# Optimization experiments

Measured on AMD Instinct MI355X. Metric: run time of the kernel, lower is better.

Reference implementation:

```python
import jax, jax.numpy as jnp
import numpy as np

B, N, M = 8, 8192, 2048
C, CP = 256, 256          # num_features, num_features_prev
D1, D2 = 256, 256         # layer_dims
BN_EPS = 1e-5


def setup_inputs() -> dict:
    key = jax.random.key(0)
    ks = jax.random.split(key, 8)
    return {
        "xyz": jax.random.normal(ks[0], (B, N, 3), dtype=jnp.float32),
        "xyz_prev": jax.random.normal(ks[1], (B, M, 3), dtype=jnp.float32),
        "features": jax.random.normal(ks[2], (B, C, N), dtype=jnp.float32),
        "features_prev": jax.random.normal(ks[3], (B, CP, M), dtype=jnp.float32),
        "w1": jax.random.normal(ks[4], (D1, C + CP), dtype=jnp.float32) * 0.02,
        "b1": jnp.zeros((D1,), dtype=jnp.float32),
        "g1": jnp.ones((D1,), dtype=jnp.float32),
        "beta1": jnp.zeros((D1,), dtype=jnp.float32),
        "w2": jax.random.normal(ks[5], (D2, D1), dtype=jnp.float32) * 0.02,
        "b2": jnp.zeros((D2,), dtype=jnp.float32),
        "g2": jnp.ones((D2,), dtype=jnp.float32),
        "beta2": jnp.zeros((D2,), dtype=jnp.float32),
    }


def _three_nn(unknown, known):
    # squared pairwise distances via GEMM form: [B, n, m]
    sq_u = jnp.sum(unknown * unknown, axis=-1)          # [B, n]
    sq_k = jnp.sum(known * known, axis=-1)              # [B, m]
    d2 = sq_u[:, :, None] + sq_k[:, None, :] - 2.0 * jnp.einsum(
        "bnd,bmd->bnm", unknown, known)
    neg_top, idx = jax.lax.top_k(-d2, 3)                # 3 smallest, ascending
    dist = jnp.sqrt(jnp.maximum(-neg_top, 0.0))         # [B, n, 3]
    return dist, idx


def _three_interpolate(features, idx, weight):
    # features [B, c, m], idx [B, n, 3], weight [B, n, 3] -> [B, c, n]
    gathered = jax.vmap(lambda f, i: f[:, i])(features, idx)  # [B, c, n, 3]
    return jnp.einsum("bcnk,bnk->bcn", gathered, weight)


def _bn_relu(x, gamma, beta):
    # training-mode BatchNorm1d over (batch, points), biased variance
    mean = jnp.mean(x, axis=(0, 2), keepdims=True)
    var = jnp.var(x, axis=(0, 2), keepdims=True)
    xh = (x - mean) * jax.lax.rsqrt(var + BN_EPS)
    return jnp.maximum(xh * gamma[None, :, None] + beta[None, :, None], 0.0)


def reference(xyz, xyz_prev, features, features_prev,
              w1, b1, g1, beta1, w2, b2, g2, beta2):
    dist, idx = _three_nn(xyz, xyz_prev)
    inv = 1.0 / (dist + 1e-8)
    weights = inv / jnp.sum(inv, axis=2, keepdims=True)           # [B, n, 3]
    new_features = _three_interpolate(features_prev, idx, weights)  # [B, cp, n]
    x = jnp.concatenate([new_features, features], axis=1)           # [B, cp+c, n]
    x = _bn_relu(jnp.einsum("oi,bin->bon", w1, x) + b1[None, :, None], g1, beta1)
    x = _bn_relu(jnp.einsum("oi,bin->bon", w2, x) + b2[None, :, None], g2, beta2)
    return x
```

## Files before the change

kernel.cpp:

```cpp
#include <hip/hip_runtime.h>

#define BDIM 8
#define NPTS 8192
#define MPTS 2048
#define NCHUNK 8
#define CHSZ 256
#define NSAMP 65536.0f
#define PITCH 40

typedef __attribute__((ext_vector_type(8))) short bf16x8;
typedef __attribute__((ext_vector_type(4))) float f32x4;

static __device__ __forceinline__ unsigned short f2bf(float f) {
  unsigned int x = __float_as_uint(f);
  x += 0x7FFFu + ((x >> 16) & 1u);
  return (unsigned short)(x >> 16);
}
static __device__ __forceinline__ float bf2f(unsigned short u) {
  return __uint_as_float(((unsigned int)u) << 16);
}

__global__ __launch_bounds__(256, 8)
void prep_kernel(const float* __restrict__ xyz, const float* __restrict__ xyz_prev,
                 float4* __restrict__ pd, int4* __restrict__ pi,
                 const float* __restrict__ features, unsigned short* __restrict__ Xf,
                 const float* __restrict__ features_prev, unsigned short* __restrict__ fpT,
                 const float* __restrict__ w1, const float* __restrict__ w2,
                 unsigned short* __restrict__ w1b, unsigned short* __restrict__ w2b) {
  __shared__ __align__(16) char smem[9216];
  const int tid = threadIdx.x;
  const int grp = blockIdx.x / 31, slot = blockIdx.x % 31;

  if (slot < 8) {
    const int id = grp*8 + slot;
    float4* pk = (float4*)smem;
    const int ch = (id >> 5) & 7, b = id >> 8;
    const int mbase = ch*CHSZ;
    {
      const int j = mbase + tid;
      float x = xyz_prev[((size_t)b*MPTS + j)*3 + 0];
      float y = xyz_prev[((size_t)b*MPTS + j)*3 + 1];
      float z = xyz_prev[((size_t)b*MPTS + j)*3 + 2];
      float s = __fadd_rn(__fadd_rn(__fmul_rn(x,x), __fmul_rn(y,y)), __fmul_rn(z,z));
      pk[tid] = make_float4(x, y, z, s);
    }
    __syncthreads();
    const int n = (id & 31)*256 + tid;
    const size_t qoff = ((size_t)b*NPTS + n)*3;
    const float qx = xyz[qoff], qy = xyz[qoff+1], qz = xyz[qoff+2];
    const float squ = __fadd_rn(__fadd_rn(__fmul_rn(qx,qx), __fmul_rn(qy,qy)), __fmul_rn(qz,qz));

    float d0 = 3.4e38f, d1 = 3.4e38f, d2v = 3.4e38f;
    int j0 = 0, j1 = 0, j2 = 0;
    for (int m = 0; m < CHSZ; m += 16) {
      float dd[16];
      #pragma unroll
      for (int u = 0; u < 16; ++u) {
        const float4 p = pk[m + u];
        float dot = __fadd_rn(__fadd_rn(__fmul_rn(qx,p.x), __fmul_rn(qy,p.y)), __fmul_rn(qz,p.z));
        dd[u] = __fsub_rn(__fadd_rn(squ, p.w), __fmul_rn(2.0f, dot));
      }
      float mn = dd[0];
      #pragma unroll
      for (int u = 1; u < 16; ++u) mn = fminf(mn, dd[u]);
      if (mn < d2v) {
        #pragma unroll
        for (int u = 0; u < 16; ++u) {
          const float v = dd[u];
          if (v < d2v) {
            if (v < d1) {
              d2v = d1; j2 = j1;
              if (v < d0) { d1 = d0; j1 = j0; d0 = v; j0 = mbase + m + u; }
              else        { d1 = v;  j1 = mbase + m + u; }
            } else { d2v = v; j2 = mbase + m + u; }
          }
        }
      }
    }
    const size_t q = (size_t)b*NPTS + n;
    pd[(size_t)ch*(BDIM*NPTS) + q] = make_float4(d0, d1, d2v, 0.f);
    pi[(size_t)ch*(BDIM*NPTS) + q] = make_int4(j0, j1, j2, 0);

  } else if (slot < 24) {
    const int id = grp*16 + (slot - 8);
    unsigned short (*St)[72] = (unsigned short(*)[72])smem;
    const int n0 = (id & 127)*64, c0 = ((id >> 7) & 3)*64, b = id >> 9;
    const int cl = tid >> 2;
    #pragma unroll
    for (int i = 0; i < 4; ++i) {
      int nl = (tid & 3)*16 + i*4;
      float4 v = *(const float4*)&features[((size_t)(b*256 + c0 + cl))*NPTS + n0 + nl];
      St[cl][nl]   = f2bf(v.x); St[cl][nl+1] = f2bf(v.y);
      St[cl][nl+2] = f2bf(v.z); St[cl][nl+3] = f2bf(v.w);
    }
    __syncthreads();
    #pragma unroll
    for (int i = 0; i < 2; ++i) {
      int u = tid + i*256;
      int nl = u >> 3, c8 = (u & 7)*8;
      unsigned short tmp[8];
      #pragma unroll
      for (int j = 0; j < 8; ++j) tmp[j] = St[c8 + j][nl];
      *(uint4*)&Xf[((size_t)(b*NPTS + n0 + nl))*256 + c0 + c8] = *(uint4*)tmp;
    }

  } else if (slot < 28) {
    const int id = grp*4 + (slot - 24);
    unsigned short (*St)[72] = (unsigned short(*)[72])smem;
    const int n0 = (id & 31)*64, c0 = ((id >> 5) & 3)*64, b = id >> 7;
    const int cl = tid >> 2;
    #pragma unroll
    for (int i = 0; i < 4; ++i) {
      int nl = (tid & 3)*16 + i*4;
      float4 v = *(const float4*)&features_prev[((size_t)(b*256 + c0 + cl))*MPTS + n0 + nl];
      St[cl][nl]   = f2bf(v.x); St[cl][nl+1] = f2bf(v.y);
      St[cl][nl+2] = f2bf(v.z); St[cl][nl+3] = f2bf(v.w);
    }
    __syncthreads();
    #pragma unroll
    for (int i = 0; i < 2; ++i) {
      int u = tid + i*256;
      int nl = u >> 3, c8 = (u & 7)*8;
      unsigned short tmp[8];
      #pragma unroll
      for (int j = 0; j < 8; ++j) tmp[j] = St[c8 + j][nl];
      *(uint4*)&fpT[((size_t)(b*MPTS + n0 + nl))*256 + c0 + c8] = *(uint4*)tmp;
    }

  } else {
    const int id = grp*3 + (slot - 28);
    const int t = id*256 + tid;
    if (t < 131072) w1b[t] = f2bf(w1[t]);
    else            w2b[t - 131072] = f2bf(w2[t - 131072]);
  }
}

__global__ __launch_bounds__(256)
void nn_merge_kernel(const float4* __restrict__ pd, const int4* __restrict__ pi,
                     int* __restrict__ idx_out, float* __restrict__ wgt_out) {
  const size_t q = (size_t)blockIdx.x*256 + threadIdx.x;
  float d0 = 3.4e38f, d1 = 3.4e38f, d2v = 3.4e38f;
  int j0 = 0, j1 = 0, j2 = 0;
  #pragma unroll
  for (int c = 0; c < NCHUNK; ++c) {
    const float4 dv = pd[(size_t)c*(BDIM*NPTS) + q];
    const int4   iv = pi[(size_t)c*(BDIM*NPTS) + q];
    const float dl[3] = {dv.x, dv.y, dv.z};
    const int   jl[3] = {iv.x, iv.y, iv.z};
    #pragma unroll
    for (int t = 0; t < 3; ++t) {
      const float v = dl[t]; const int j = jl[t];
      if (v < d2v) {
        if (v < d1) {
          d2v = d1; j2 = j1;
          if (v < d0) { d1 = d0; j1 = j0; d0 = v; j0 = j; }
          else        { d1 = v;  j1 = j; }
        } else { d2v = v; j2 = j; }
      }
    }
  }
  const float s0 = sqrtf(fmaxf(d0, 0.f));
  const float s1 = sqrtf(fmaxf(d1, 0.f));
  const float s2 = sqrtf(fmaxf(d2v, 0.f));
  const float i0 = 1.f/(s0 + 1e-8f), i1 = 1.f/(s1 + 1e-8f), i2 = 1.f/(s2 + 1e-8f);
  const float sum = i0 + i1 + i2;
  idx_out[q*3] = j0; idx_out[q*3+1] = j1; idx_out[q*3+2] = j2;
  wgt_out[q*3] = i0/sum; wgt_out[q*3+1] = i1/sum; wgt_out[q*3+2] = i2/sum;
}

__global__ __launch_bounds__(512)
void gemm1_fused_kernel(const unsigned short* __restrict__ W,
                        const unsigned short* __restrict__ Xf,
                        const unsigned short* __restrict__ fpT,
                        const int* __restrict__ idx, const float* __restrict__ wgt,
                        const float* __restrict__ bias,
                        unsigned short* __restrict__ Y, float* __restrict__ part) {
  __shared__ __align__(16) unsigned short Ws[256*PITCH];
  __shared__ __align__(16) unsigned short Xs[128*PITCH];
  __shared__ float lsum[256], lsq[256];
  const int tid = threadIdx.x;
  const int b = blockIdx.y, n0 = blockIdx.x*128;
  const int row = tid >> 2, seg = tid & 3;

  if (tid < 256) { lsum[tid] = 0.f; lsq[tid] = 0.f; }

  const size_t p = ((size_t)b*NPTS + n0 + row)*3;
  const int   i0 = idx[p],  i1 = idx[p+1],  i2 = idx[p+2];
  const float w0 = wgt[p],  w1 = wgt[p+1],  w2 = wgt[p+2];
  const unsigned short* fb  = fpT + (size_t)b*MPTS*256;
  const unsigned short* Xfb = Xf  + ((size_t)(b*NPTS + n0) + row)*256;

  uint4 wv0 = *(const uint4*)&W[(size_t)row*512 + seg*8];
  uint4 wv1 = *(const uint4*)&W[(size_t)(row+128)*512 + seg*8];
  uint4 xv;
  {
    const int k0 = seg*8;
    uint4 a0 = *(const uint4*)&fb[(size_t)i0*256 + k0];
    uint4 a1 = *(const uint4*)&fb[(size_t)i1*256 + k0];
    uint4 a2 = *(const uint4*)&fb[(size_t)i2*256 + k0];
    const unsigned short* u0 = (const unsigned short*)&a0;
    const unsigned short* u1 = (const unsigned short*)&a1;
    const unsigned short* u2 = (const unsigned short*)&a2;
    unsigned short r[8];
    #pragma unroll
    for (int j = 0; j < 8; ++j)
      r[j] = f2bf(bf2f(u0[j])*w0 + bf2f(u1[j])*w1 + bf2f(u2[j])*w2);
    xv = *(uint4*)r;
  }

  f32x4 acc[4][4];
  #pragma unroll
  for (int i = 0; i < 4; ++i)
    #pragma unroll
    for (int j = 0; j < 4; ++j) acc[i][j] = (f32x4){0.f,0.f,0.f,0.f};

  const int lane = tid & 63, l16 = lane & 15, quad = lane >> 4;
  const int wave = tid >> 6, wo = wave >> 1, wn = wave & 1;

  for (int kt = 0; kt < 16; ++kt) {
    __syncthreads();
    *(uint4*)&Ws[row*PITCH + seg*8]       = wv0;
    *(uint4*)&Ws[(row+128)*PITCH + seg*8] = wv1;
    *(uint4*)&Xs[row*PITCH + seg*8]       = xv;
    __syncthreads();
    if (kt + 1 < 16) {
      const int k0 = (kt+1)*32;
      wv0 = *(const uint4*)&W[(size_t)row*512 + k0 + seg*8];
      wv1 = *(const uint4*)&W[(size_t)(row+128)*512 + k0 + seg*8];
      const int kx = k0 + seg*8;
      if (kx < 256) {
        uint4 a0 = *(const uint4*)&fb[(size_t)i0*256 + kx];
        uint4 a1 = *(const uint4*)&fb[(size_t)i1*256 + kx];
        uint4 a2 = *(const uint4*)&fb[(size_t)i2*256 + kx];
        const unsigned short* u0 = (const unsigned short*)&a0;
        const unsigned short* u1 = (const unsigned short*)&a1;
        const unsigned short* u2 = (const unsigned short*)&a2;
        unsigned short r[8];
        #pragma unroll
        for (int j = 0; j < 8; ++j)
          r[j] = f2bf(bf2f(u0[j])*w0 + bf2f(u1[j])*w1 + bf2f(u2[j])*w2);
        xv = *(uint4*)r;
      } else {
        xv = *(const uint4*)&Xfb[kx - 256];
      }
    }
    bf16x8 af[4], bfr[4];
    #pragma unroll
    for (int to = 0; to < 4; ++to)
      af[to] = *(const bf16x8*)&Ws[(wo*64 + to*16 + l16)*PITCH + quad*8];
    #pragma unroll
    for (int tn = 0; tn < 4; ++tn)
      bfr[tn] = *(const bf16x8*)&Xs[(wn*64 + tn*16 + l16)*PITCH + quad*8];
    #pragma unroll
    for (int to = 0; to < 4; ++to)
      #pragma unroll
      for (int tn = 0; tn < 4; ++tn)
        acc[to][tn] = __builtin_amdgcn_mfma_f32_16x16x32_bf16(af[to], bfr[tn], acc[to][tn], 0, 0, 0);
  }

  #pragma unroll
  for (int to = 0; to < 4; ++to) {
    #pragma unroll
    for (int r = 0; r < 4; ++r) {
      const int o = wo*64 + to*16 + quad*4 + r;
      const float bv = bias[o];
      float ps = 0.f, qs = 0.f;
      #pragma unroll
      for (int tn = 0; tn < 4; ++tn) {
        float v = acc[to][tn][r] + bv;
        acc[to][tn][r] = v;
        ps += v; qs = fmaf(v, v, qs);
      }
      #pragma unroll
      for (int m = 1; m < 16; m <<= 1) { ps += __shfl_xor(ps, m); qs += __shfl_xor(qs, m); }
      if (l16 == 0) { atomicAdd(&lsum[o], ps); atomicAdd(&lsq[o], qs); }
    }
  }
  #pragma unroll
  for (int to = 0; to < 4; ++to)
    #pragma unroll
    for (int tn = 0; tn < 4; ++tn) {
      const int n = n0 + wn*64 + tn*16 + l16;
      const int o = wo*64 + to*16 + quad*4;
      unsigned int lo = (unsigned)f2bf(acc[to][tn][0]) | ((unsigned)f2bf(acc[to][tn][1]) << 16);
      unsigned int hi = (unsigned)f2bf(acc[to][tn][2]) | ((unsigned)f2bf(acc[to][tn][3]) << 16);
      *(uint2*)&Y[((size_t)(b*NPTS + n))*256 + o] = make_uint2(lo, hi);
    }
  __syncthreads();
  if (tid < 256) {
    const int blk = b*gridDim.x + blockIdx.x;
    part[(size_t)blk*512 + tid]       = lsum[tid];
    part[(size_t)blk*512 + 256 + tid] = lsq[tid];
  }
}

template<int KD, int MODE>
__global__ __launch_bounds__(512)
void gemm_t_kernel(const unsigned short* __restrict__ W, const unsigned short* __restrict__ X,
                   const float* __restrict__ bias, const float* __restrict__ scl,
                   const float* __restrict__ shf, unsigned short* __restrict__ Y,
                   float* __restrict__ part) {
  __shared__ __align__(16) unsigned short Ws[256*PITCH];
  __shared__ __align__(16) unsigned short Xs[128*PITCH];
  __shared__ float lsum[256], lsq[256];
  const int tid = threadIdx.x;
  const int b = blockIdx.y, n0 = blockIdx.x*128;
  const int row = tid >> 2, seg = tid & 3;
  const unsigned short* Xb = X + (size_t)(b*NPTS + n0)*KD;

  if (tid < 256) { lsum[tid] = 0.f; lsq[tid] = 0.f; }

  uint4 wv0 = *(const uint4*)&W[(size_t)row*KD + seg*8];
  uint4 wv1 = *(const uint4*)&W[(size_t)(row+128)*KD + seg*8];
  uint4 xv  = *(const uint4*)&Xb[(size_t)row*KD + seg*8];

  f32x4 acc[4][4];
  #pragma unroll
  for (int i = 0; i < 4; ++i)
    #pragma unroll
    for (int j = 0; j < 4; ++j) acc[i][j] = (f32x4){0.f,0.f,0.f,0.f};

  const int lane = tid & 63, l16 = lane & 15, quad = lane >> 4;
  const int wave = tid >> 6, wo = wave >> 1, wn = wave & 1;

  for (int kt = 0; kt < KD/32; ++kt) {
    __syncthreads();
    *(uint4*)&Ws[row*PITCH + seg*8]       = wv0;
    *(uint4*)&Ws[(row+128)*PITCH + seg*8] = wv1;
    if (MODE == 0) {
      *(uint4*)&Xs[row*PITCH + seg*8] = xv;
    } else {
      const int kc = kt*32 + seg*8;
      float4 s0 = *(const float4*)&scl[kc], s1 = *(const float4*)&scl[kc+4];
      float4 h0 = *(const float4*)&shf[kc], h1 = *(const float4*)&shf[kc+4];
      const unsigned short* xu = (const unsigned short*)&xv;
      unsigned short t[8];
      t[0] = f2bf(fmaxf(fmaf(bf2f(xu[0]), s0.x, h0.x), 0.f));
      t[1] = f2bf(fmaxf(fmaf(bf2f(xu[1]), s0.y, h0.y), 0.f));
      t[2] = f2bf(fmaxf(fmaf(bf2f(xu[2]), s0.z, h0.z), 0.f));
      t[3] = f2bf(fmaxf(fmaf(bf2f(xu[3]), s0.w, h0.w), 0.f));
      t[4] = f2bf(fmaxf(fmaf(bf2f(xu[4]), s1.x, h1.x), 0.f));
      t[5] = f2bf(fmaxf(fmaf(bf2f(xu[5]), s1.y, h1.y), 0.f));
      t[6] = f2bf(fmaxf(fmaf(bf2f(xu[6]), s1.z, h1.z), 0.f));
      t[7] = f2bf(fmaxf(fmaf(bf2f(xu[7]), s1.w, h1.w), 0.f));
      *(uint4*)&Xs[row*PITCH + seg*8] = *(uint4*)t;
    }
    __syncthreads();
    if (kt + 1 < KD/32) {
      const int k0 = (kt+1)*32;
      wv0 = *(const uint4*)&W[(size_t)row*KD + k0 + seg*8];
      wv1 = *(const uint4*)&W[(size_t)(row+128)*KD + k0 + seg*8];
      xv  = *(const uint4*)&Xb[(size_t)row*KD + k0 + seg*8];
    }
    bf16x8 af[4], bfr[4];
    #pragma unroll
    for (int to = 0; to < 4; ++to)
      af[to] = *(const bf16x8*)&Ws[(wo*64 + to*16 + l16)*PITCH + quad*8];
    #pragma unroll
    for (int tn = 0; tn < 4; ++tn)
      bfr[tn] = *(const bf16x8*)&Xs[(wn*64 + tn*16 + l16)*PITCH + quad*8];
    #pragma unroll
    for (int to = 0; to < 4; ++to)
      #pragma unroll
      for (int tn = 0; tn < 4; ++tn)
        acc[to][tn] = __builtin_amdgcn_mfma_f32_16x16x32_bf16(af[to], bfr[tn], acc[to][tn], 0, 0, 0);
  }

  #pragma unroll
  for (int to = 0; to < 4; ++to) {
    #pragma unroll
    for (int r = 0; r < 4; ++r) {
      const int o = wo*64 + to*16 + quad*4 + r;
      const float bv = bias[o];
      float p = 0.f, q = 0.f;
      #pragma unroll
      for (int tn = 0; tn < 4; ++tn) {
        float v = acc[to][tn][r] + bv;
        acc[to][tn][r] = v;
        p += v; q = fmaf(v, v, q);
      }
      #pragma unroll
      for (int m = 1; m < 16; m <<= 1) { p += __shfl_xor(p, m); q += __shfl_xor(q, m); }
      if (l16 == 0) { atomicAdd(&lsum[o], p); atomicAdd(&lsq[o], q); }
    }
  }
  #pragma unroll
  for (int to = 0; to < 4; ++to)
    #pragma unroll
    for (int tn = 0; tn < 4; ++tn) {
      const int n = n0 + wn*64 + tn*16 + l16;
      const int o = wo*64 + to*16 + quad*4;
      unsigned int lo = (unsigned)f2bf(acc[to][tn][0]) | ((unsigned)f2bf(acc[to][tn][1]) << 16);
      unsigned int hi = (unsigned)f2bf(acc[to][tn][2]) | ((unsigned)f2bf(acc[to][tn][3]) << 16);
      *(uint2*)&Y[((size_t)(b*NPTS + n))*256 + o] = make_uint2(lo, hi);
    }
  __syncthreads();
  if (tid < 256) {
    const int blk = b*gridDim.x + blockIdx.x;
    part[(size_t)blk*512 + tid]       = lsum[tid];
    part[(size_t)blk*512 + 256 + tid] = lsq[tid];
  }
}

__global__ __launch_bounds__(256)
void bn_reduce_kernel(const float* __restrict__ part, const float* __restrict__ g,
                      const float* __restrict__ beta, float* __restrict__ scl,
                      float* __restrict__ shf) {
  __shared__ float ls[4], lq[4];
  const int o = blockIdx.x;
  const int t = threadIdx.x;
  float s = part[(size_t)t*512 + o]        + part[(size_t)(t+256)*512 + o];
  float q = part[(size_t)t*512 + 256 + o]  + part[(size_t)(t+256)*512 + 256 + o];
  #pragma unroll
  for (int m = 1; m < 64; m <<= 1) { s += __shfl_xor(s, m); q += __shfl_xor(q, m); }
  const int w = t >> 6;
  if ((t & 63) == 0) { ls[w] = s; lq[w] = q; }
  __syncthreads();
  if (t == 0) {
    const float ss = ls[0] + ls[1] + ls[2] + ls[3];
    const float qq = lq[0] + lq[1] + lq[2] + lq[3];
    const float inv_n = 1.0f / NSAMP;
    const float mean = ss * inv_n;
    const float var  = qq * inv_n - mean*mean;
    const float sc = g[o] * rsqrtf(var + 1e-5f);
    scl[o] = sc;
    shf[o] = beta[o] - mean * sc;
  }
}

__global__ __launch_bounds__(256)
void bn2_t_kernel(const unsigned short* __restrict__ Yt, const float* __restrict__ scl,
                  const float* __restrict__ shf, float* __restrict__ out) {
  __shared__ __align__(16) unsigned short T[64][72];
  const int tid = threadIdx.x;
  const int n0 = blockIdx.x*64, o0 = blockIdx.y*64, b = blockIdx.z;
  #pragma unroll
  for (int i = 0; i < 2; ++i) {
    int u = tid + i*256;
    int nl = u >> 3, o8 = (u & 7)*8;
    uint4 v = *(const uint4*)&Yt[((size_t)(b*NPTS + n0 + nl))*256 + o0 + o8];
    *(uint4*)&T[nl][o8] = v;
  }
  __syncthreads();
  #pragma unroll
  for (int i = 0; i < 4; ++i) {
    int u = tid + i*256;
    int ol = u >> 4, n4 = (u & 15)*4;
    const float s = scl[o0+ol], h = shf[o0+ol];
    float4 v;
    v.x = fmaxf(fmaf(bf2f(T[n4  ][ol]), s, h), 0.f);
    v.y = fmaxf(fmaf(bf2f(T[n4+1][ol]), s, h), 0.f);
    v.z = fmaxf(fmaf(bf2f(T[n4+2][ol]), s, h), 0.f);
    v.w = fmaxf(fmaf(bf2f(T[n4+3][ol]), s, h), 0.f);
    *(float4*)&out[((size_t)(b*256 + o0 + ol))*NPTS + n0 + n4] = v;
  }
}

extern "C" void kernel_launch(void* const* d_in, const int* in_sizes, int n_in,
                              void* d_out, int out_size, void* d_ws, size_t ws_size,
                              hipStream_t stream) {
  const float* xyz           = (const float*)d_in[0];
  const float* xyz_prev      = (const float*)d_in[1];
  const float* features      = (const float*)d_in[2];
  const float* features_prev = (const float*)d_in[3];
  const float* w1    = (const float*)d_in[4];
  const float* b1    = (const float*)d_in[5];
  const float* g1    = (const float*)d_in[6];
  const float* beta1 = (const float*)d_in[7];
  const float* w2    = (const float*)d_in[8];
  const float* b2    = (const float*)d_in[9];
  const float* g2    = (const float*)d_in[10];
  const float* beta2 = (const float*)d_in[11];
  float* out = (float*)d_out;

  char* ws = (char*)d_ws;
  int*            idxb = (int*)ws;
  float*          wgtb = (float*)(ws + 786432);
  float*          bn   = (float*)(ws + 1572864);
  unsigned short* w1b  = (unsigned short*)(ws + 1581056);
  unsigned short* w2b  = (unsigned short*)(ws + 1843200);
  unsigned short* Xf   = (unsigned short*)(ws + 2097152);
  unsigned short* y2t  = Xf;
  unsigned short* y1t  = (unsigned short*)d_out;
  unsigned short* fpT  = (unsigned short*)((char*)d_out + 33554432);
  float*          part = (float*)((char*)d_out + 41943040);
  float4*         pd   = (float4*)((char*)d_out + 46137344);
  int4*           pi   = (int4*)((char*)d_out + 54525952);

  float* bn1_scl = bn;        float* bn1_shf = bn + 256;
  float* bn2_scl = bn + 512;  float* bn2_shf = bn + 768;

  prep_kernel<<<7936, 256, 0, stream>>>(xyz, xyz_prev, pd, pi,
                                        features, Xf, features_prev, fpT,
                                        w1, w2, w1b, w2b);
  nn_merge_kernel<<<(BDIM*NPTS)/256, 256, 0, stream>>>(pd, pi, idxb, wgtb);

  gemm1_fused_kernel<<<dim3(NPTS/128, BDIM), 512, 0, stream>>>(
      w1b, Xf, fpT, idxb, wgtb, b1, y1t, part);
  bn_reduce_kernel<<<256, 256, 0, stream>>>(part, g1, beta1, bn1_scl, bn1_shf);

  gemm_t_kernel<256, 1><<<dim3(NPTS/128, BDIM), 512, 0, stream>>>(
      w2b, y1t, b2, bn1_scl, bn1_shf, y2t, part);
  bn_reduce_kernel<<<256, 256, 0, stream>>>(part, g2, beta2, bn2_scl, bn2_shf);

  bn2_t_kernel<<<dim3(NPTS/64, 4, BDIM), 256, 0, stream>>>(y2t, bn2_scl, bn2_shf, out);
}
```

Measured before the change: 285.4 us.

## Fold NN merge into GEMM1 and coarsen prep transpose blocks

Drops the separate nn_merge kernel: GEMM1 now merges the per-chunk top-3 candidates and computes the inverse-distance weights inline from pd/pi, which removes one launch and the idx/wgt round trip through memory. The prep kernel's transpose blocks each handle four tiles instead of one, so the grid shrinks from 7936 to 3584 blocks. The shared tile pitch changes from 72 to 65 to reduce bank conflicts on the transposed reads. In exchange, every GEMM1 thread loads 8 float4+int4 pairs and runs the merge, and each transpose block has less parallelism, with extra syncs between its tiles.

```diff
diff --git a/kernel.cpp b/kernel.cpp
--- a/kernel.cpp
+++ b/kernel.cpp
@@ -7,6 +7,7 @@
 #define CHSZ 256
 #define NSAMP 65536.0f
 #define PITCH 40
+#define TP 65
 
 typedef __attribute__((ext_vector_type(8))) short bf16x8;
 typedef __attribute__((ext_vector_type(4))) float f32x4;
@@ -27,9 +28,9 @@
                  const float* __restrict__ features_prev, unsigned short* __restrict__ fpT,
                  const float* __restrict__ w1, const float* __restrict__ w2,
                  unsigned short* __restrict__ w1b, unsigned short* __restrict__ w2b) {
-  __shared__ __align__(16) char smem[9216];
+  __shared__ __align__(16) char smem[8448];
   const int tid = threadIdx.x;
-  const int grp = blockIdx.x / 31, slot = blockIdx.x % 31;
+  const int grp = blockIdx.x / 14, slot = blockIdx.x % 14;
 
   if (slot < 8) {
     const int id = grp*8 + slot;
@@ -81,98 +82,75 @@
     pd[(size_t)ch*(BDIM*NPTS) + q] = make_float4(d0, d1, d2v, 0.f);
     pi[(size_t)ch*(BDIM*NPTS) + q] = make_int4(j0, j1, j2, 0);
 
-  } else if (slot < 24) {
-    const int id = grp*16 + (slot - 8);
-    unsigned short (*St)[72] = (unsigned short(*)[72])smem;
-    const int n0 = (id & 127)*64, c0 = ((id >> 7) & 3)*64, b = id >> 9;
-    const int cl = tid >> 2;
-    #pragma unroll
-    for (int i = 0; i < 4; ++i) {
-      int nl = (tid & 3)*16 + i*4;
-      float4 v = *(const float4*)&features[((size_t)(b*256 + c0 + cl))*NPTS + n0 + nl];
-      St[cl][nl]   = f2bf(v.x); St[cl][nl+1] = f2bf(v.y);
-      St[cl][nl+2] = f2bf(v.z); St[cl][nl+3] = f2bf(v.w);
-    }
-    __syncthreads();
-    #pragma unroll
-    for (int i = 0; i < 2; ++i) {
-      int u = tid + i*256;
-      int nl = u >> 3, c8 = (u & 7)*8;
-      unsigned short tmp[8];
-      #pragma unroll
-      for (int j = 0; j < 8; ++j) tmp[j] = St[c8 + j][nl];
-      *(uint4*)&Xf[((size_t)(b*NPTS + n0 + nl))*256 + c0 + c8] = *(uint4*)tmp;
-    }
-
-  } else if (slot < 28) {
-    const int id = grp*4 + (slot - 24);
-    unsigned short (*St)[72] = (unsigned short(*)[72])smem;
-    const int n0 = (id & 31)*64, c0 = ((id >> 5) & 3)*64, b = id >> 7;
-    const int cl = tid >> 2;
-    #pragma unroll
-    for (int i = 0; i < 4; ++i) {
-      int nl = (tid & 3)*16 + i*4;
-      float4 v = *(const float4*)&features_prev[((size_t)(b*256 + c0 + cl))*MPTS + n0 + nl];
-      St[cl][nl]   = f2bf(v.x); St[cl][nl+1] = f2bf(v.y);
-      St[cl][nl+2] = f2bf(v.z); St[cl][nl+3] = f2bf(v.w);
-    }
-    __syncthreads();
-    #pragma unroll
-    for (int i = 0; i < 2; ++i) {
-      int u = tid + i*256;
-      int nl = u >> 3, c8 = (u & 7)*8;
-      unsigned short tmp[8];
-      #pragma unroll
-      for (int j = 0; j < 8; ++j) tmp[j] = St[c8 + j][nl];
-      *(uint4*)&fpT[((size_t)(b*MPTS + n0 + nl))*256 + c0 + c8] = *(uint4*)tmp;
+  } else if (slot < 12) {
+    unsigned short (*St)[TP] = (unsigned short(*)[TP])smem;
+    const int base = (grp*4 + (slot - 8))*4;
+    for (int t = 0; t < 4; ++t) {
+      const int id = base + t;
+      const int n0 = (id & 127)*64, c0 = ((id >> 7) & 3)*64, b = id >> 9;
+      const int cl = tid >> 2;
+      if (t) __syncthreads();
+      #pragma unroll
+      for (int i = 0; i < 4; ++i) {
+        int nl = (tid & 3)*16 + i*4;
+        float4 v = *(const float4*)&features[((size_t)(b*256 + c0 + cl))*NPTS + n0 + nl];
+        St[cl][nl]   = f2bf(v.x); St[cl][nl+1] = f2bf(v.y);
+        St[cl][nl+2] = f2bf(v.z); St[cl][nl+3] = f2bf(v.w);
+      }
+      __syncthreads();
+      #pragma unroll
+      for (int i = 0; i < 2; ++i) {
+        int u = tid + i*256;
+        int nl = u >> 3, c8 = (u & 7)*8;
+        unsigned short tmp[8];
+        #pragma unroll
+        for (int j = 0; j < 8; ++j) tmp[j] = St[c8 + j][nl];
+        *(uint4*)&Xf[((size_t)(b*NPTS + n0 + nl))*256 + c0 + c8] = *(uint4*)tmp;
+      }
+    }
+
+  } else if (slot < 13) {
+    unsigned short (*St)[TP] = (unsigned short(*)[TP])smem;
+    const int base = grp*4;
+    for (int t = 0; t < 4; ++t) {
+      const int id = base + t;
+      const int n0 = (id & 31)*64, c0 = ((id >> 5) & 3)*64, b = id >> 7;
+      const int cl = tid >> 2;
+      if (t) __syncthreads();
+      #pragma unroll
+      for (int i = 0; i < 4; ++i) {
+        int nl = (tid & 3)*16 + i*4;
+        float4 v = *(const float4*)&features_prev[((size_t)(b*256 + c0 + cl))*MPTS + n0 + nl];
+        St[cl][nl]   = f2bf(v.x); St[cl][nl+1] = f2bf(v.y);
+        St[cl][nl+2] = f2bf(v.z); St[cl][nl+3] = f2bf(v.w);
+      }
+      __syncthreads();
+      #pragma unroll
+      for (int i = 0; i < 2; ++i) {
+        int u = tid + i*256;
+        int nl = u >> 3, c8 = (u & 7)*8;
+        unsigned short tmp[8];
+        #pragma unroll
+        for (int j = 0; j < 8; ++j) tmp[j] = St[c8 + j][nl];
+        *(uint4*)&fpT[((size_t)(b*MPTS + n0 + nl))*256 + c0 + c8] = *(uint4*)tmp;
+      }
     }
 
   } else {
-    const int id = grp*3 + (slot - 28);
-    const int t = id*256 + tid;
-    if (t < 131072) w1b[t] = f2bf(w1[t]);
-    else            w2b[t - 131072] = f2bf(w2[t - 131072]);
-  }
-}
-
-__global__ __launch_bounds__(256)
-void nn_merge_kernel(const float4* __restrict__ pd, const int4* __restrict__ pi,
-                     int* __restrict__ idx_out, float* __restrict__ wgt_out) {
-  const size_t q = (size_t)blockIdx.x*256 + threadIdx.x;
-  float d0 = 3.4e38f, d1 = 3.4e38f, d2v = 3.4e38f;
-  int j0 = 0, j1 = 0, j2 = 0;
-  #pragma unroll
-  for (int c = 0; c < NCHUNK; ++c) {
-    const float4 dv = pd[(size_t)c*(BDIM*NPTS) + q];
-    const int4   iv = pi[(size_t)c*(BDIM*NPTS) + q];
-    const float dl[3] = {dv.x, dv.y, dv.z};
-    const int   jl[3] = {iv.x, iv.y, iv.z};
-    #pragma unroll
-    for (int t = 0; t < 3; ++t) {
-      const float v = dl[t]; const int j = jl[t];
-      if (v < d2v) {
-        if (v < d1) {
-          d2v = d1; j2 = j1;
-          if (v < d0) { d1 = d0; j1 = j0; d0 = v; j0 = j; }
-          else        { d1 = v;  j1 = j; }
-        } else { d2v = v; j2 = j; }
-      }
-    }
-  }
-  const float s0 = sqrtf(fmaxf(d0, 0.f));
-  const float s1 = sqrtf(fmaxf(d1, 0.f));
-  const float s2 = sqrtf(fmaxf(d2v, 0.f));
-  const float i0 = 1.f/(s0 + 1e-8f), i1 = 1.f/(s1 + 1e-8f), i2 = 1.f/(s2 + 1e-8f);
-  const float sum = i0 + i1 + i2;
-  idx_out[q*3] = j0; idx_out[q*3+1] = j1; idx_out[q*3+2] = j2;
-  wgt_out[q*3] = i0/sum; wgt_out[q*3+1] = i1/sum; wgt_out[q*3+2] = i2/sum;
+    #pragma unroll
+    for (int k = 0; k < 3; ++k) {
+      const int t = (grp*3 + k)*256 + tid;
+      if (t < 131072) w1b[t] = f2bf(w1[t]);
+      else            w2b[t - 131072] = f2bf(w2[t - 131072]);
+    }
+  }
 }
 
 __global__ __launch_bounds__(512)
 void gemm1_fused_kernel(const unsigned short* __restrict__ W,
                         const unsigned short* __restrict__ Xf,
                         const unsigned short* __restrict__ fpT,
-                        const int* __restrict__ idx, const float* __restrict__ wgt,
+                        const float4* __restrict__ pd, const int4* __restrict__ pi,
                         const float* __restrict__ bias,
                         unsigned short* __restrict__ Y, float* __restrict__ part) {
   __shared__ __align__(16) unsigned short Ws[256*PITCH];
@@ -184,9 +162,37 @@
 
   if (tid < 256) { lsum[tid] = 0.f; lsq[tid] = 0.f; }
 
-  const size_t p = ((size_t)b*NPTS + n0 + row)*3;
-  const int   i0 = idx[p],  i1 = idx[p+1],  i2 = idx[p+2];
-  const float w0 = wgt[p],  w1 = wgt[p+1],  w2 = wgt[p+2];
+  int i0, i1, i2; float w0, w1, w2;
+  {
+    const size_t q = (size_t)b*NPTS + n0 + row;
+    float d0 = 3.4e38f, d1 = 3.4e38f, d2v = 3.4e38f;
+    int j0 = 0, j1 = 0, j2 = 0;
+    #pragma unroll
+    for (int c = 0; c < NCHUNK; ++c) {
+      const float4 dv = pd[(size_t)c*(BDIM*NPTS) + q];
+      const int4   iv = pi[(size_t)c*(BDIM*NPTS) + q];
+      const float dl[3] = {dv.x, dv.y, dv.z};
+      const int   jl[3] = {iv.x, iv.y, iv.z};
+      #pragma unroll
+      for (int t = 0; t < 3; ++t) {
+        const float v = dl[t]; const int j = jl[t];
+        if (v < d2v) {
+          if (v < d1) {
+            d2v = d1; j2 = j1;
+            if (v < d0) { d1 = d0; j1 = j0; d0 = v; j0 = j; }
+            else        { d1 = v;  j1 = j; }
+          } else { d2v = v; j2 = j; }
+        }
+      }
+    }
+    const float s0 = sqrtf(fmaxf(d0, 0.f));
+    const float s1 = sqrtf(fmaxf(d1, 0.f));
+    const float s2 = sqrtf(fmaxf(d2v, 0.f));
+    const float r0 = 1.f/(s0 + 1e-8f), r1 = 1.f/(s1 + 1e-8f), r2 = 1.f/(s2 + 1e-8f);
+    const float sum = r0 + r1 + r2;
+    i0 = j0; i1 = j1; i2 = j2;
+    w0 = r0/sum; w1 = r1/sum; w2 = r2/sum;
+  }
   const unsigned short* fb  = fpT + (size_t)b*MPTS*256;
   const unsigned short* Xfb = Xf  + ((size_t)(b*NPTS + n0) + row)*256;
 
@@ -474,8 +480,6 @@
   float* out = (float*)d_out;
 
   char* ws = (char*)d_ws;
-  int*            idxb = (int*)ws;
-  float*          wgtb = (float*)(ws + 786432);
   float*          bn   = (float*)(ws + 1572864);
   unsigned short* w1b  = (unsigned short*)(ws + 1581056);
   unsigned short* w2b  = (unsigned short*)(ws + 1843200);
@@ -490,13 +494,12 @@
   float* bn1_scl = bn;        float* bn1_shf = bn + 256;
   float* bn2_scl = bn + 512;  float* bn2_shf = bn + 768;
 
-  prep_kernel<<<7936, 256, 0, stream>>>(xyz, xyz_prev, pd, pi,
+  prep_kernel<<<3584, 256, 0, stream>>>(xyz, xyz_prev, pd, pi,
                                         features, Xf, features_prev, fpT,
                                         w1, w2, w1b, w2b);
-  nn_merge_kernel<<<(BDIM*NPTS)/256, 256, 0, stream>>>(pd, pi, idxb, wgtb);
 
   gemm1_fused_kernel<<<dim3(NPTS/128, BDIM), 512, 0, stream>>>(
-      w1b, Xf, fpT, idxb, wgtb, b1, y1t, part);
+      w1b, Xf, fpT, pd, pi, b1, y1t, part);
   bn_reduce_kernel<<<256, 256, 0, stream>>>(part, g1, beta1, bn1_scl, bn1_shf);
 
   gemm_t_kernel<256, 1><<<dim3(NPTS/128, BDIM), 512, 0, stream>>>(
```

After: 280.1 us. No clear change (-1.8%).
